# Optimization experiments

Measured on AMD Instinct MI355X. Metric: run time of the kernel, lower is better.

## Reference

```python
import jax, jax.numpy as jnp
import numpy as np

VOCAB = 40
BATCH = 262144
SEQLEN = 128


def setup_inputs() -> dict:
    key = jax.random.key(0)
    x = jax.random.randint(key, (BATCH, SEQLEN), 0, VOCAB, dtype=jnp.int32)
    return {"x": x}


def reference(x) -> jnp.ndarray:
    # x: [B, L] int token ids; 0 is padding (excluded from stats).
    B = x.shape[0]
    valid = (x != 0).astype(jnp.float32)  # [B, L]
    # Per-row histogram via scatter-add; pad positions scatter 0.0 into bin 0.
    rows = jnp.arange(B, dtype=jnp.int32)[:, None]
    counts = jnp.zeros((B, VOCAB), jnp.float32).at[rows, x].add(valid)  # [B, V]
    total = counts.sum(axis=-1, keepdims=True)  # [B, 1]
    nonempty = total[:, 0] > 0  # [B]
    probs = counts / jnp.maximum(total, 1.0)  # [B, V]
    pos = counts > 0
    unique = pos.sum(axis=-1).astype(jnp.float32) / VOCAB  # unique_chars / vocab
    max_freq = probs.max(axis=-1)
    min_freq = jnp.where(pos, probs, jnp.inf).min(axis=-1)
    min_freq = jnp.where(nonempty, min_freq, 0.0)
    letter_ratio = probs[:, 1:27].sum(axis=-1)
    digit_ratio = probs[:, 27:37].sum(axis=-1)
    special_ratio = probs[:, 37:].sum(axis=-1)
    feats = jnp.stack(
        [unique, max_freq, min_freq, letter_ratio, digit_ratio, special_ratio],
        axis=-1,
    )  # [B, 6]
    # Rows with no valid (nonzero) tokens produce all-zero features.
    return jnp.where(nonempty[:, None], feats, 0.0)
```

## Files before the change

kernel.cpp:

```cpp
#include <hip/hip_runtime.h>

#define VOCAB 40
#define SEQ 128
#define THREADS 256
#define HSTRIDE 11

__global__ __launch_bounds__(THREADS) void char_dist_kernel(
    const int* __restrict__ x, float* __restrict__ out, int batch) {
  __shared__ unsigned int hist[THREADS * HSTRIDE];
  const int tid = threadIdx.x;
  const int row = blockIdx.x * THREADS + tid;
  if (row >= batch) return;

  unsigned int* h = &hist[tid * HSTRIDE];
#pragma unroll
  for (int w = 0; w < 10; ++w) h[w] = 0u;

  const int4* rowp = reinterpret_cast<const int4*>(x + (long)row * SEQ);
#pragma unroll 4
  for (int j = 0; j < SEQ / 4; ++j) {
    int4 t = rowp[j];
    int v;
    v = t.x; h[v >> 2] += 1u << ((v & 3) << 3);
    v = t.y; h[v >> 2] += 1u << ((v & 3) << 3);
    v = t.z; h[v >> 2] += 1u << ((v & 3) << 3);
    v = t.w; h[v >> 2] += 1u << ((v & 3) << 3);
  }

  int total = 0, uniq = 0, maxc = 0, minc = 256;
  int letters = 0, digits = 0, special = 0;
#pragma unroll
  for (int w = 0; w < 10; ++w) {
    unsigned int word = h[w];
#pragma unroll
    for (int b = 0; b < 4; ++b) {
      const int v = w * 4 + b;
      if (v == 0) continue;
      if (v >= VOCAB) continue;
      int c = (int)((word >> (b * 8)) & 0xFFu);
      total += c;
      uniq += (c > 0) ? 1 : 0;
      maxc = max(maxc, c);
      if (c > 0) minc = min(minc, c);
      if (v <= 26) letters += c;
      else if (v <= 36) digits += c;
      else special += c;
    }
  }

  float f0, f1, f2, f3, f4, f5;
  if (total > 0) {
    float inv = 1.0f / (float)total;
    f0 = (float)uniq * (1.0f / (float)VOCAB);
    f1 = (float)maxc * inv;
    f2 = (float)minc * inv;
    f3 = (float)letters * inv;
    f4 = (float)digits * inv;
    f5 = (float)special * inv;
  } else {
    f0 = f1 = f2 = f3 = f4 = f5 = 0.0f;
  }

  float2* o = reinterpret_cast<float2*>(out + (long)row * 6);
  o[0] = make_float2(f0, f1);
  o[1] = make_float2(f2, f3);
  o[2] = make_float2(f4, f5);
}

extern "C" void kernel_launch(void* const* d_in, const int* in_sizes, int n_in,
                              void* d_out, int out_size, void* d_ws, size_t ws_size,
                              hipStream_t stream) {
  const int* x = (const int*)d_in[0];
  float* out = (float*)d_out;
  const int batch = in_sizes[0] / SEQ;
  const int blocks = (batch + THREADS - 1) / THREADS;
  char_dist_kernel<<<blocks, THREADS, 0, stream>>>(x, out, batch);
}
```

Baseline: 194.0 us.

## Split each row across two threads with dual sub-histograms and shuffle reduction

Each row is now processed by a pair of threads, each reading half the row, so twice as many threads are in flight and each thread's sequential loads shrink. Each thread keeps two interleaved packed sub-histograms to break LDS read-modify-write dependency chains, and the explicit loads are software-prefetched. The pair merges histograms through shared memory after a barrier, splits the bin scan, and combines statistics with xor shuffles. This raises LDS use per block and adds a block barrier.

```diff
diff --git a/kernel.cpp b/kernel.cpp
--- a/kernel.cpp
+++ b/kernel.cpp
@@ -3,68 +3,108 @@
 #define VOCAB 40
 #define SEQ 128
 #define THREADS 256
-#define HSTRIDE 11
+#define ROWS_PER_BLOCK (THREADS / 2)
+#define HW 21
 
 __global__ __launch_bounds__(THREADS) void char_dist_kernel(
     const int* __restrict__ x, float* __restrict__ out, int batch) {
-  __shared__ unsigned int hist[THREADS * HSTRIDE];
+  __shared__ unsigned int hist[THREADS * HW];
   const int tid = threadIdx.x;
-  const int row = blockIdx.x * THREADS + tid;
-  if (row >= batch) return;
+  const int row = blockIdx.x * ROWS_PER_BLOCK + (tid >> 1);
+  const int half = tid & 1;
+  const bool active = row < batch;
 
-  unsigned int* h = &hist[tid * HSTRIDE];
+  unsigned int* h = &hist[tid * HW];
 #pragma unroll
-  for (int w = 0; w < 10; ++w) h[w] = 0u;
+  for (int w = 0; w < 20; ++w) h[w] = 0u;
 
-  const int4* rowp = reinterpret_cast<const int4*>(x + (long)row * SEQ);
-#pragma unroll 4
-  for (int j = 0; j < SEQ / 4; ++j) {
-    int4 t = rowp[j];
-    int v;
-    v = t.x; h[v >> 2] += 1u << ((v & 3) << 3);
-    v = t.y; h[v >> 2] += 1u << ((v & 3) << 3);
-    v = t.z; h[v >> 2] += 1u << ((v & 3) << 3);
-    v = t.w; h[v >> 2] += 1u << ((v & 3) << 3);
+  if (active) {
+    const int4* rowp = reinterpret_cast<const int4*>(x) +
+                       ((long)row * (SEQ / 4) + half * (SEQ / 8));
+    int4 c0 = rowp[0], c1 = rowp[1], c2 = rowp[2], c3 = rowp[3];
+#pragma unroll
+    for (int j = 0; j < 16; j += 4) {
+      int4 n0 = c0, n1 = c1, n2 = c2, n3 = c3;
+      if (j + 4 < 16) {
+        n0 = rowp[j + 4];
+        n1 = rowp[j + 5];
+        n2 = rowp[j + 6];
+        n3 = rowp[j + 7];
+      }
+      h[c0.x >> 2] += 1u << ((c0.x & 3) << 3);
+      h[10 + (c0.y >> 2)] += 1u << ((c0.y & 3) << 3);
+      h[c0.z >> 2] += 1u << ((c0.z & 3) << 3);
+      h[10 + (c0.w >> 2)] += 1u << ((c0.w & 3) << 3);
+
+      h[c1.x >> 2] += 1u << ((c1.x & 3) << 3);
+      h[10 + (c1.y >> 2)] += 1u << ((c1.y & 3) << 3);
+      h[c1.z >> 2] += 1u << ((c1.z & 3) << 3);
+      h[10 + (c1.w >> 2)] += 1u << ((c1.w & 3) << 3);
+
+      h[c2.x >> 2] += 1u << ((c2.x & 3) << 3);
+      h[10 + (c2.y >> 2)] += 1u << ((c2.y & 3) << 3);
+      h[c2.z >> 2] += 1u << ((c2.z & 3) << 3);
+      h[10 + (c2.w >> 2)] += 1u << ((c2.w & 3) << 3);
+
+      h[c3.x >> 2] += 1u << ((c3.x & 3) << 3);
+      h[10 + (c3.y >> 2)] += 1u << ((c3.y & 3) << 3);
+      h[c3.z >> 2] += 1u << ((c3.z & 3) << 3);
+      h[10 + (c3.w >> 2)] += 1u << ((c3.w & 3) << 3);
+
+      c0 = n0; c1 = n1; c2 = n2; c3 = n3;
+    }
   }
+  __syncthreads();
 
-  int total = 0, uniq = 0, maxc = 0, minc = 256;
+  const unsigned int* hp = &hist[(tid ^ 1) * HW];
+  int total = 0, uniq = 0, maxc = 0, minc = 0x7fffffff;
   int letters = 0, digits = 0, special = 0;
+  const int wbase = half * 5;
 #pragma unroll
-  for (int w = 0; w < 10; ++w) {
-    unsigned int word = h[w];
+  for (int k = 0; k < 5; ++k) {
+    const int w = wbase + k;
+    const unsigned int m = h[w] + h[10 + w] + hp[w] + hp[10 + w];
 #pragma unroll
     for (int b = 0; b < 4; ++b) {
-      const int v = w * 4 + b;
-      if (v == 0) continue;
-      if (v >= VOCAB) continue;
-      int c = (int)((word >> (b * 8)) & 0xFFu);
-      total += c;
-      uniq += (c > 0) ? 1 : 0;
-      maxc = max(maxc, c);
-      if (c > 0) minc = min(minc, c);
-      if (v <= 26) letters += c;
-      else if (v <= 36) digits += c;
-      else special += c;
+      const int bin = w * 4 + b;
+      const int c = (int)((m >> (b * 8)) & 0xFFu);
+      if (bin != 0) {
+        total += c;
+        uniq += (c > 0) ? 1 : 0;
+        maxc = max(maxc, c);
+        if (c > 0) minc = min(minc, c);
+        if (bin <= 26) letters += c;
+        else if (bin <= 36) digits += c;
+        else special += c;
+      }
     }
   }
 
-  float f0, f1, f2, f3, f4, f5;
-  if (total > 0) {
-    float inv = 1.0f / (float)total;
-    f0 = (float)uniq * (1.0f / (float)VOCAB);
-    f1 = (float)maxc * inv;
-    f2 = (float)minc * inv;
-    f3 = (float)letters * inv;
-    f4 = (float)digits * inv;
-    f5 = (float)special * inv;
-  } else {
-    f0 = f1 = f2 = f3 = f4 = f5 = 0.0f;
+  total   += __shfl_xor(total, 1);
+  uniq    += __shfl_xor(uniq, 1);
+  letters += __shfl_xor(letters, 1);
+  digits  += __shfl_xor(digits, 1);
+  special += __shfl_xor(special, 1);
+  maxc = max(maxc, __shfl_xor(maxc, 1));
+  minc = min(minc, __shfl_xor(minc, 1));
+
+  if (active) {
+    if (minc == 0x7fffffff) minc = 0;
+    const float inv = 1.0f / (float)max(total, 1);
+    const float f0 = (float)uniq * (1.0f / (float)VOCAB);
+    const float f1 = (float)maxc * inv;
+    const float f2 = (float)minc * inv;
+    const float f3 = (float)letters * inv;
+    const float f4 = (float)digits * inv;
+    const float f5 = (float)special * inv;
+    float2* o = reinterpret_cast<float2*>(out + (long)row * 6);
+    if (half == 0) {
+      o[0] = make_float2(f0, f1);
+      o[1] = make_float2(f2, f3);
+    } else {
+      o[2] = make_float2(f4, f5);
+    }
   }
-
-  float2* o = reinterpret_cast<float2*>(out + (long)row * 6);
-  o[0] = make_float2(f0, f1);
-  o[1] = make_float2(f2, f3);
-  o[2] = make_float2(f4, f5);
 }
 
 extern "C" void kernel_launch(void* const* d_in, const int* in_sizes, int n_in,
@@ -73,6 +113,6 @@
   const int* x = (const int*)d_in[0];
   float* out = (float*)d_out;
   const int batch = in_sizes[0] / SEQ;
-  const int blocks = (batch + THREADS - 1) / THREADS;
+  const int blocks = (batch + ROWS_PER_BLOCK - 1) / ROWS_PER_BLOCK;
   char_dist_kernel<<<blocks, THREADS, 0, stream>>>(x, out, batch);
 }
```

After: 204.2 us. 1.05x slower.

## Stage row tiles through LDS with coalesced loads and register double-buffering

Applied to the files above, without the earlier changes.

Rather than each thread reading its own 512-byte row with strided int4 loads, groups of 8 threads now cooperatively load 128-byte row chunks in a coalesced pattern. The chunks are staged into a padded shared-memory tile and each thread then reads its own row back from LDS. Two register buffers let the next chunk's global loads be issued before the current chunk is stored and processed. The goal is better global-memory coalescing, at the cost of extra LDS traffic, more shared memory per block (hurting occupancy) and several __syncthreads barriers.

```diff
diff --git a/kernel.cpp b/kernel.cpp
--- a/kernel.cpp
+++ b/kernel.cpp
@@ -3,54 +3,96 @@
 #define VOCAB 40
 #define SEQ 128
 #define THREADS 256
-#define HSTRIDE 11
+#define RSTRIDE 36
+#define HW 11
 
 __global__ __launch_bounds__(THREADS) void char_dist_kernel(
     const int* __restrict__ x, float* __restrict__ out, int batch) {
-  __shared__ unsigned int hist[THREADS * HSTRIDE];
+  __shared__ unsigned int tile[THREADS * RSTRIDE];
+  __shared__ unsigned int hist[THREADS * HW];
   const int tid = threadIdx.x;
-  const int row = blockIdx.x * THREADS + tid;
-  if (row >= batch) return;
+  const int rowBase = blockIdx.x * THREADS;
 
-  unsigned int* h = &hist[tid * HSTRIDE];
+  unsigned int* h = &hist[tid * HW];
 #pragma unroll
   for (int w = 0; w < 10; ++w) h[w] = 0u;
 
-  const int4* rowp = reinterpret_cast<const int4*>(x + (long)row * SEQ);
-#pragma unroll 4
-  for (int j = 0; j < SEQ / 4; ++j) {
-    int4 t = rowp[j];
-    int v;
-    v = t.x; h[v >> 2] += 1u << ((v & 3) << 3);
-    v = t.y; h[v >> 2] += 1u << ((v & 3) << 3);
-    v = t.z; h[v >> 2] += 1u << ((v & 3) << 3);
-    v = t.w; h[v >> 2] += 1u << ((v & 3) << 3);
+  const int lrow = tid >> 3;
+  const int lblk = tid & 7;
+  const int4* gbase = reinterpret_cast<const int4*>(x);
+
+#define LOAD_CHUNK(R, c)                                                     \
+  _Pragma("unroll") for (int k = 0; k < 8; ++k) {                            \
+    const int r = k * 32 + lrow;                                             \
+    const long grow = (long)(rowBase + r);                                   \
+    (R)[k] = (grow < batch) ? gbase[grow * 32 + (c) * 8 + lblk]              \
+                            : make_int4(0, 0, 0, 0);                         \
   }
 
-  int total = 0, uniq = 0, maxc = 0, minc = 256;
+#define STORE_CHUNK(R)                                                       \
+  _Pragma("unroll") for (int k = 0; k < 8; ++k) {                            \
+    const int r = k * 32 + lrow;                                             \
+    *reinterpret_cast<int4*>(&tile[r * RSTRIDE + lblk * 4]) = (R)[k];        \
+  }
+
+#define PROC_CHUNK()                                                         \
+  _Pragma("unroll") for (int k = 0; k < 8; ++k) {                            \
+    const int4 t4 =                                                          \
+        *reinterpret_cast<const int4*>(&tile[tid * RSTRIDE + k * 4]);        \
+    h[t4.x >> 2] += 1u << ((t4.x & 3) << 3);                                 \
+    h[t4.y >> 2] += 1u << ((t4.y & 3) << 3);                                 \
+    h[t4.z >> 2] += 1u << ((t4.z & 3) << 3);                                 \
+    h[t4.w >> 2] += 1u << ((t4.w & 3) << 3);                                 \
+  }
+
+  int4 A[8], B[8];
+  LOAD_CHUNK(A, 0)
+  LOAD_CHUNK(B, 1)
+  STORE_CHUNK(A)
+  __syncthreads();
+  PROC_CHUNK()
+  __syncthreads();
+  LOAD_CHUNK(A, 2)
+  STORE_CHUNK(B)
+  __syncthreads();
+  PROC_CHUNK()
+  __syncthreads();
+  LOAD_CHUNK(B, 3)
+  STORE_CHUNK(A)
+  __syncthreads();
+  PROC_CHUNK()
+  __syncthreads();
+  STORE_CHUNK(B)
+  __syncthreads();
+  PROC_CHUNK()
+
+  const int row = rowBase + tid;
+  if (row >= batch) return;
+
+  int total = 0, uniq = 0, maxc = 0, minc = 0x7fffffff;
   int letters = 0, digits = 0, special = 0;
 #pragma unroll
   for (int w = 0; w < 10; ++w) {
-    unsigned int word = h[w];
+    const unsigned int m = h[w];
 #pragma unroll
     for (int b = 0; b < 4; ++b) {
-      const int v = w * 4 + b;
-      if (v == 0) continue;
-      if (v >= VOCAB) continue;
-      int c = (int)((word >> (b * 8)) & 0xFFu);
-      total += c;
-      uniq += (c > 0) ? 1 : 0;
-      maxc = max(maxc, c);
-      if (c > 0) minc = min(minc, c);
-      if (v <= 26) letters += c;
-      else if (v <= 36) digits += c;
-      else special += c;
+      const int bin = w * 4 + b;
+      const int c = (int)((m >> (b * 8)) & 0xFFu);
+      if (bin != 0) {
+        total += c;
+        uniq += (c > 0) ? 1 : 0;
+        maxc = max(maxc, c);
+        if (c > 0) minc = min(minc, c);
+        if (bin <= 26) letters += c;
+        else if (bin <= 36) digits += c;
+        else special += c;
+      }
     }
   }
 
   float f0, f1, f2, f3, f4, f5;
   if (total > 0) {
-    float inv = 1.0f / (float)total;
+    const float inv = 1.0f / (float)total;
     f0 = (float)uniq * (1.0f / (float)VOCAB);
     f1 = (float)maxc * inv;
     f2 = (float)minc * inv;
@@ -60,7 +102,6 @@
   } else {
     f0 = f1 = f2 = f3 = f4 = f5 = 0.0f;
   }
-
   float2* o = reinterpret_cast<float2*>(out + (long)row * 6);
   o[0] = make_float2(f0, f1);
   o[1] = make_float2(f2, f3);
```

After: 192.1 us. Within noise of the previous version (-1.0%).
